# Performance work log

Hardware: AMD Instinct MI355X
Metric: run time of the kernel (lower is better)

## Reference

```python
import jax, jax.numpy as jnp
import numpy as np

B, T, C = 1, 2_000_000, 16
NAN_FRAC = 0.05  # fraction of entries replaced by NaN, as the layer is a NaN-interpolation op


def setup_inputs() -> dict:
    key = jax.random.key(0)
    k_x, k_m = jax.random.split(key)
    x = jax.random.normal(k_x, (B, T, C), dtype=jnp.float32)
    nan_mask = jax.random.uniform(k_m, (B, T, C)) < NAN_FRAC
    x = jnp.where(nan_mask, jnp.float32(jnp.nan), x)
    return {"inputs": x}


def reference(inputs):
    # Vectorized form of the per-column loop: for each column, compute the
    # mean of the valid (non-NaN) entries along time and fill NaNs with it.
    # (Original code computes this per column with tf.reduce_mean + tf.map_fn
    # + tf.where/tf.fill; here it is a single fused pass.)
    mask = jnp.isnan(inputs)                       # [B, T, C]
    safe = jnp.where(mask, jnp.float32(0.0), inputs)
    valid = jnp.sum(jnp.logical_not(mask).astype(inputs.dtype), axis=1)  # [B, C]
    mean = jnp.sum(safe, axis=1) / jnp.maximum(valid, 1.0)               # [B, C]
    out = jnp.where(mask, mean[:, None, :], safe)  # broadcast NaN fill
    return out
```

## Files before the change

### kernel.cpp

```cpp
#include <hip/hip_runtime.h>

#define C_COLS 16

__global__ __launch_bounds__(256) void k_reduce(const float4* __restrict__ x4,
                                                long long n4,
                                                float* __restrict__ partials) {
    const int tid = threadIdx.x;
    const long long gid = (long long)blockIdx.x * blockDim.x + tid;
    const long long stride = (long long)gridDim.x * blockDim.x;

    float s0 = 0.f, s1 = 0.f, s2 = 0.f, s3 = 0.f;
    float c0 = 0.f, c1 = 0.f, c2 = 0.f, c3 = 0.f;

    for (long long i = gid; i < n4; i += stride) {
        float4 v = x4[i];
        bool m0 = (v.x == v.x); s0 += m0 ? v.x : 0.f; c0 += m0 ? 1.f : 0.f;
        bool m1 = (v.y == v.y); s1 += m1 ? v.y : 0.f; c1 += m1 ? 1.f : 0.f;
        bool m2 = (v.z == v.z); s2 += m2 ? v.z : 0.f; c2 += m2 ? 1.f : 0.f;
        bool m3 = (v.w == v.w); s3 += m3 ? v.w : 0.f; c3 += m3 ? 1.f : 0.f;
    }

    for (int off = 4; off < 64; off <<= 1) {
        s0 += __shfl_xor(s0, off, 64);
        s1 += __shfl_xor(s1, off, 64);
        s2 += __shfl_xor(s2, off, 64);
        s3 += __shfl_xor(s3, off, 64);
        c0 += __shfl_xor(c0, off, 64);
        c1 += __shfl_xor(c1, off, 64);
        c2 += __shfl_xor(c2, off, 64);
        c3 += __shfl_xor(c3, off, 64);
    }

    __shared__ float bsum[C_COLS];
    __shared__ float bcnt[C_COLS];
    if (tid < C_COLS) { bsum[tid] = 0.f; bcnt[tid] = 0.f; }
    __syncthreads();

    if ((tid & 63) < 4) {
        const int cb = (tid & 3) * 4;
        atomicAdd(&bsum[cb + 0], s0);
        atomicAdd(&bsum[cb + 1], s1);
        atomicAdd(&bsum[cb + 2], s2);
        atomicAdd(&bsum[cb + 3], s3);
        atomicAdd(&bcnt[cb + 0], c0);
        atomicAdd(&bcnt[cb + 1], c1);
        atomicAdd(&bcnt[cb + 2], c2);
        atomicAdd(&bcnt[cb + 3], c3);
    }
    __syncthreads();

    if (tid < C_COLS) {
        partials[(long long)blockIdx.x * 32 + tid] = bsum[tid];
        partials[(long long)blockIdx.x * 32 + 16 + tid] = bcnt[tid];
    }
}

__global__ __launch_bounds__(256) void k_final(const float* __restrict__ partials,
                                               int nb,
                                               const float* __restrict__ x,
                                               long long n4, long long n,
                                               float* __restrict__ mean_out) {
    const int tid = threadIdx.x;
    const int c = tid & 15;
    const int r0 = tid >> 4;

    float s = 0.f, cnt = 0.f;
    for (int p = r0; p < nb; p += 16) {
        s   += partials[(long long)p * 32 + c];
        cnt += partials[(long long)p * 32 + 16 + c];
    }

    __shared__ float ssum[256];
    __shared__ float scnt[256];
    ssum[tid] = s;
    scnt[tid] = cnt;
    __syncthreads();

    if (tid < 16) {
        float S = 0.f, Cn = 0.f;
        for (int r = 0; r < 16; ++r) {
            S  += ssum[r * 16 + tid];
            Cn += scnt[r * 16 + tid];
        }
        for (long long j = n4 * 4; j < n; ++j) {
            if ((int)(j % 16) == tid) {
                float v = x[j];
                if (v == v) { S += v; Cn += 1.f; }
            }
        }
        mean_out[tid] = S / fmaxf(Cn, 1.f);
    }
}

__global__ __launch_bounds__(256) void k_fill(const float4* __restrict__ x4,
                                              float4* __restrict__ o4,
                                              long long n4, long long n,
                                              const float* __restrict__ mean) {
    const int tid = threadIdx.x;
    const long long gid = (long long)blockIdx.x * blockDim.x + tid;
    const long long stride = (long long)gridDim.x * blockDim.x;

    const int cb = (int)(gid & 3) * 4;
    const float m0 = mean[cb + 0];
    const float m1 = mean[cb + 1];
    const float m2 = mean[cb + 2];
    const float m3 = mean[cb + 3];

    for (long long i = gid; i < n4; i += stride) {
        float4 v = x4[i];
        v.x = (v.x == v.x) ? v.x : m0;
        v.y = (v.y == v.y) ? v.y : m1;
        v.z = (v.z == v.z) ? v.z : m2;
        v.w = (v.w == v.w) ? v.w : m3;
        o4[i] = v;
    }

    if (blockIdx.x == 0 && tid == 0) {
        const float* x = (const float*)x4;
        float* o = (float*)o4;
        for (long long j = n4 * 4; j < n; ++j) {
            float v = x[j];
            o[j] = (v == v) ? v : mean[(int)(j % 16)];
        }
    }
}

extern "C" void kernel_launch(void* const* d_in, const int* in_sizes, int n_in,
                              void* d_out, int out_size, void* d_ws, size_t ws_size,
                              hipStream_t stream) {
    const float* x = (const float*)d_in[0];
    float* out = (float*)d_out;
    const long long n = (long long)in_sizes[0];
    const long long n4 = n / 4;

    int nb1 = 1024;
    {
        long long cap = ((long long)(ws_size / 4) - 16) / 32;
        if (cap < 1) cap = 1;
        if (nb1 > cap) nb1 = (int)cap;
    }
    float* partials = (float*)d_ws;
    float* mean = partials + (long long)nb1 * 32;

    k_reduce<<<nb1, 256, 0, stream>>>((const float4*)x, n4, partials);
    k_final<<<1, 256, 0, stream>>>(partials, nb1, x, n4, n, mean);

    const int nb3 = 2048;
    k_fill<<<nb3, 256, 0, stream>>>((const float4*)x, (float4*)out, n4, n, mean);
}
```

Measured before the change: 251.5 us.

## Fuse reduce, finalize and fill into one persistent kernel with grid barrier

Replaces the three kernels with one: each of 512 blocks reduces a contiguous chunk, the last block to arrive (atomic ticket) computes the column means, and all blocks spin-wait on a flag before filling the same chunk. The intent is to remove launch gaps and let the second read of each chunk hit in cache (128 MB input may partly stay in the large last-level cache). It relies on all 512 blocks being co-resident; if they are not, the spin-wait deadlocks. Loads are also unrolled by four.

```diff
diff --git a/kernel.cpp b/kernel.cpp
--- a/kernel.cpp
+++ b/kernel.cpp
@@ -1,23 +1,61 @@
 #include <hip/hip_runtime.h>
 
+#define NB 512
+#define NT 256
 #define C_COLS 16
 
-__global__ __launch_bounds__(256) void k_reduce(const float4* __restrict__ x4,
-                                                long long n4,
-                                                float* __restrict__ partials) {
+__global__ void k_init(int* __restrict__ sync) {
+    sync[0] = 0;
+    sync[1] = 0;
+}
+
+__global__ __launch_bounds__(NT, 4) void k_fused(const float4* __restrict__ x4,
+                                                 float4* __restrict__ o4,
+                                                 long long n4, long long n,
+                                                 long long chunk,
+                                                 float* __restrict__ partials,
+                                                 float* __restrict__ meanbuf,
+                                                 int* __restrict__ sync) {
     const int tid = threadIdx.x;
-    const long long gid = (long long)blockIdx.x * blockDim.x + tid;
-    const long long stride = (long long)gridDim.x * blockDim.x;
+    const int b = blockIdx.x;
+    const long long beg = (long long)b * chunk;
+    long long end = beg + chunk;
+    if (end > n4) end = n4;
 
     float s0 = 0.f, s1 = 0.f, s2 = 0.f, s3 = 0.f;
     float c0 = 0.f, c1 = 0.f, c2 = 0.f, c3 = 0.f;
 
-    for (long long i = gid; i < n4; i += stride) {
+    long long i = beg + tid;
+    for (; i + 3 * NT < end; i += 4 * NT) {
+        float4 a = x4[i];
+        float4 bb = x4[i + NT];
+        float4 cc = x4[i + 2 * NT];
+        float4 dd = x4[i + 3 * NT];
+        bool m;
+        m = (a.x == a.x);  s0 += m ? a.x : 0.f;  c0 += m ? 1.f : 0.f;
+        m = (a.y == a.y);  s1 += m ? a.y : 0.f;  c1 += m ? 1.f : 0.f;
+        m = (a.z == a.z);  s2 += m ? a.z : 0.f;  c2 += m ? 1.f : 0.f;
+        m = (a.w == a.w);  s3 += m ? a.w : 0.f;  c3 += m ? 1.f : 0.f;
+        m = (bb.x == bb.x); s0 += m ? bb.x : 0.f; c0 += m ? 1.f : 0.f;
+        m = (bb.y == bb.y); s1 += m ? bb.y : 0.f; c1 += m ? 1.f : 0.f;
+        m = (bb.z == bb.z); s2 += m ? bb.z : 0.f; c2 += m ? 1.f : 0.f;
+        m = (bb.w == bb.w); s3 += m ? bb.w : 0.f; c3 += m ? 1.f : 0.f;
+        m = (cc.x == cc.x); s0 += m ? cc.x : 0.f; c0 += m ? 1.f : 0.f;
+        m = (cc.y == cc.y); s1 += m ? cc.y : 0.f; c1 += m ? 1.f : 0.f;
+        m = (cc.z == cc.z); s2 += m ? cc.z : 0.f; c2 += m ? 1.f : 0.f;
+        m = (cc.w == cc.w); s3 += m ? cc.w : 0.f; c3 += m ? 1.f : 0.f;
+        m = (dd.x == dd.x); s0 += m ? dd.x : 0.f; c0 += m ? 1.f : 0.f;
+        m = (dd.y == dd.y); s1 += m ? dd.y : 0.f; c1 += m ? 1.f : 0.f;
+        m = (dd.z == dd.z); s2 += m ? dd.z : 0.f; c2 += m ? 1.f : 0.f;
+        m = (dd.w == dd.w); s3 += m ? dd.w : 0.f; c3 += m ? 1.f : 0.f;
+    }
+    for (; i < end; i += NT) {
         float4 v = x4[i];
-        bool m0 = (v.x == v.x); s0 += m0 ? v.x : 0.f; c0 += m0 ? 1.f : 0.f;
-        bool m1 = (v.y == v.y); s1 += m1 ? v.y : 0.f; c1 += m1 ? 1.f : 0.f;
-        bool m2 = (v.z == v.z); s2 += m2 ? v.z : 0.f; c2 += m2 ? 1.f : 0.f;
-        bool m3 = (v.w == v.w); s3 += m3 ? v.w : 0.f; c3 += m3 ? 1.f : 0.f;
+        bool m;
+        m = (v.x == v.x); s0 += m ? v.x : 0.f; c0 += m ? 1.f : 0.f;
+        m = (v.y == v.y); s1 += m ? v.y : 0.f; c1 += m ? 1.f : 0.f;
+        m = (v.z == v.z); s2 += m ? v.z : 0.f; c2 += m ? 1.f : 0.f;
+        m = (v.w == v.w); s3 += m ? v.w : 0.f; c3 += m ? 1.f : 0.f;
     }
 
     for (int off = 4; off < 64; off <<= 1) {
@@ -35,7 +73,6 @@
     __shared__ float bcnt[C_COLS];
     if (tid < C_COLS) { bsum[tid] = 0.f; bcnt[tid] = 0.f; }
     __syncthreads();
-
     if ((tid & 63) < 4) {
         const int cb = (tid & 3) * 4;
         atomicAdd(&bsum[cb + 0], s0);
@@ -48,65 +85,102 @@
         atomicAdd(&bcnt[cb + 3], c3);
     }
     __syncthreads();
-
     if (tid < C_COLS) {
-        partials[(long long)blockIdx.x * 32 + tid] = bsum[tid];
-        partials[(long long)blockIdx.x * 32 + 16 + tid] = bcnt[tid];
-    }
-}
-
-__global__ __launch_bounds__(256) void k_final(const float* __restrict__ partials,
-                                               int nb,
-                                               const float* __restrict__ x,
-                                               long long n4, long long n,
-                                               float* __restrict__ mean_out) {
-    const int tid = threadIdx.x;
-    const int c = tid & 15;
-    const int r0 = tid >> 4;
-
-    float s = 0.f, cnt = 0.f;
-    for (int p = r0; p < nb; p += 16) {
-        s   += partials[(long long)p * 32 + c];
-        cnt += partials[(long long)p * 32 + 16 + c];
-    }
-
-    __shared__ float ssum[256];
-    __shared__ float scnt[256];
-    ssum[tid] = s;
-    scnt[tid] = cnt;
-    __syncthreads();
-
-    if (tid < 16) {
-        float S = 0.f, Cn = 0.f;
-        for (int r = 0; r < 16; ++r) {
-            S  += ssum[r * 16 + tid];
-            Cn += scnt[r * 16 + tid];
-        }
-        for (long long j = n4 * 4; j < n; ++j) {
-            if ((int)(j % 16) == tid) {
-                float v = x[j];
-                if (v == v) { S += v; Cn += 1.f; }
+        partials[b * 32 + tid]      = bsum[tid];
+        partials[b * 32 + 16 + tid] = bcnt[tid];
+    }
+    __threadfence();
+
+    __shared__ int ticket;
+    if (tid == 0)
+        ticket = __hip_atomic_fetch_add(&sync[0], 1, __ATOMIC_ACQ_REL,
+                                        __HIP_MEMORY_SCOPE_AGENT);
+    __syncthreads();
+
+    if (ticket == NB - 1) {
+        const int c = tid & 15;
+        const int r0 = tid >> 4;
+        float s = 0.f, cn = 0.f;
+        for (int p = r0; p < NB; p += 16) {
+            s  += __hip_atomic_load(&partials[p * 32 + c], __ATOMIC_RELAXED,
+                                    __HIP_MEMORY_SCOPE_AGENT);
+            cn += __hip_atomic_load(&partials[p * 32 + 16 + c], __ATOMIC_RELAXED,
+                                    __HIP_MEMORY_SCOPE_AGENT);
+        }
+        __shared__ float ssum[NT];
+        __shared__ float scnt[NT];
+        ssum[tid] = s;
+        scnt[tid] = cn;
+        __syncthreads();
+        if (tid < 16) {
+            float S = 0.f, Cn = 0.f;
+            for (int r = 0; r < 16; ++r) {
+                S  += ssum[r * 16 + tid];
+                Cn += scnt[r * 16 + tid];
             }
-        }
-        mean_out[tid] = S / fmaxf(Cn, 1.f);
-    }
-}
-
-__global__ __launch_bounds__(256) void k_fill(const float4* __restrict__ x4,
-                                              float4* __restrict__ o4,
-                                              long long n4, long long n,
-                                              const float* __restrict__ mean) {
-    const int tid = threadIdx.x;
-    const long long gid = (long long)blockIdx.x * blockDim.x + tid;
-    const long long stride = (long long)gridDim.x * blockDim.x;
-
-    const int cb = (int)(gid & 3) * 4;
-    const float m0 = mean[cb + 0];
-    const float m1 = mean[cb + 1];
-    const float m2 = mean[cb + 2];
-    const float m3 = mean[cb + 3];
-
-    for (long long i = gid; i < n4; i += stride) {
+            const float* xs = (const float*)x4;
+            for (long long j = n4 * 4; j < n; ++j) {
+                if ((int)(j % 16) == tid) {
+                    float v = xs[j];
+                    if (v == v) { S += v; Cn += 1.f; }
+                }
+            }
+            __hip_atomic_store(&meanbuf[tid], S / fmaxf(Cn, 1.f),
+                               __ATOMIC_RELEASE, __HIP_MEMORY_SCOPE_AGENT);
+        }
+        __syncthreads();
+        __threadfence();
+        if (tid == 0)
+            __hip_atomic_store(&sync[1], 1, __ATOMIC_RELEASE,
+                               __HIP_MEMORY_SCOPE_AGENT);
+    }
+
+    if (tid == 0) {
+        while (__hip_atomic_load(&sync[1], __ATOMIC_ACQUIRE,
+                                 __HIP_MEMORY_SCOPE_AGENT) == 0) {
+            __builtin_amdgcn_s_sleep(8);
+        }
+    }
+    __syncthreads();
+
+    const int cb = (tid & 3) * 4;
+    const float m0 = __hip_atomic_load(&meanbuf[cb + 0], __ATOMIC_RELAXED,
+                                       __HIP_MEMORY_SCOPE_AGENT);
+    const float m1 = __hip_atomic_load(&meanbuf[cb + 1], __ATOMIC_RELAXED,
+                                       __HIP_MEMORY_SCOPE_AGENT);
+    const float m2 = __hip_atomic_load(&meanbuf[cb + 2], __ATOMIC_RELAXED,
+                                       __HIP_MEMORY_SCOPE_AGENT);
+    const float m3 = __hip_atomic_load(&meanbuf[cb + 3], __ATOMIC_RELAXED,
+                                       __HIP_MEMORY_SCOPE_AGENT);
+
+    i = beg + tid;
+    for (; i + 3 * NT < end; i += 4 * NT) {
+        float4 a = x4[i];
+        float4 bb = x4[i + NT];
+        float4 cc = x4[i + 2 * NT];
+        float4 dd = x4[i + 3 * NT];
+        a.x = (a.x == a.x) ? a.x : m0;
+        a.y = (a.y == a.y) ? a.y : m1;
+        a.z = (a.z == a.z) ? a.z : m2;
+        a.w = (a.w == a.w) ? a.w : m3;
+        bb.x = (bb.x == bb.x) ? bb.x : m0;
+        bb.y = (bb.y == bb.y) ? bb.y : m1;
+        bb.z = (bb.z == bb.z) ? bb.z : m2;
+        bb.w = (bb.w == bb.w) ? bb.w : m3;
+        cc.x = (cc.x == cc.x) ? cc.x : m0;
+        cc.y = (cc.y == cc.y) ? cc.y : m1;
+        cc.z = (cc.z == cc.z) ? cc.z : m2;
+        cc.w = (cc.w == cc.w) ? cc.w : m3;
+        dd.x = (dd.x == dd.x) ? dd.x : m0;
+        dd.y = (dd.y == dd.y) ? dd.y : m1;
+        dd.z = (dd.z == dd.z) ? dd.z : m2;
+        dd.w = (dd.w == dd.w) ? dd.w : m3;
+        o4[i] = a;
+        o4[i + NT] = bb;
+        o4[i + 2 * NT] = cc;
+        o4[i + 3 * NT] = dd;
+    }
+    for (; i < end; i += NT) {
         float4 v = x4[i];
         v.x = (v.x == v.x) ? v.x : m0;
         v.y = (v.y == v.y) ? v.y : m1;
@@ -115,12 +189,14 @@
         o4[i] = v;
     }
 
-    if (blockIdx.x == 0 && tid == 0) {
-        const float* x = (const float*)x4;
-        float* o = (float*)o4;
+    if (b == 0 && tid == 0) {
+        const float* xs = (const float*)x4;
+        float* os = (float*)o4;
         for (long long j = n4 * 4; j < n; ++j) {
-            float v = x[j];
-            o[j] = (v == v) ? v : mean[(int)(j % 16)];
+            float v = xs[j];
+            float mj = __hip_atomic_load(&meanbuf[(int)(j % 16)], __ATOMIC_RELAXED,
+                                         __HIP_MEMORY_SCOPE_AGENT);
+            os[j] = (v == v) ? v : mj;
         }
     }
 }
@@ -133,18 +209,13 @@
     const long long n = (long long)in_sizes[0];
     const long long n4 = n / 4;
 
-    int nb1 = 1024;
-    {
-        long long cap = ((long long)(ws_size / 4) - 16) / 32;
-        if (cap < 1) cap = 1;
-        if (nb1 > cap) nb1 = (int)cap;
-    }
     float* partials = (float*)d_ws;
-    float* mean = partials + (long long)nb1 * 32;
-
-    k_reduce<<<nb1, 256, 0, stream>>>((const float4*)x, n4, partials);
-    k_final<<<1, 256, 0, stream>>>(partials, nb1, x, n4, n, mean);
-
-    const int nb3 = 2048;
-    k_fill<<<nb3, 256, 0, stream>>>((const float4*)x, (float4*)out, n4, n, mean);
+    float* meanbuf = partials + (long long)NB * 32;
+    int* sync = (int*)(meanbuf + 16);
+
+    long long chunk = ((n4 + NB - 1) / NB + 3) & ~3LL;
+
+    k_init<<<1, 1, 0, stream>>>(sync);
+    k_fused<<<NB, NT, 0, stream>>>((const float4*)x, (float4*)out, n4, n, chunk,
+                                   partials, meanbuf, sync);
 }
```

Result: slower. 359.3 us (+42.8%).
